# Kernel optimization log

Measured on AMD Instinct MI355X. Metric: run time of the kernel, lower is better.

## Reference

```python
import jax, jax.numpy as jnp
import numpy as np

# Quincunx lattice: coset 0 at integer positions (2i, 2j), coset 1 at (2i+1, 2j+1).
# Stencil offsets in lattice coordinates (coordinate sum even -> on-lattice points).
STENCIL = [(0, 0), (1, 1), (2, 0), (0, 2), (2, 2)]
NEG_INF = -jnp.inf


def _shifted(x, di, dj):
    """Return y with y[..., i, j] = x[..., i+di, j+dj], out-of-range -> -inf."""
    H, W = x.shape[-2], x.shape[-1]
    pi0, pi1 = max(-di, 0), max(di, 0)
    pj0, pj1 = max(-dj, 0), max(dj, 0)
    xp = jnp.pad(x, ((0, 0), (0, 0), (pi0, pi1), (pj0, pj1)),
                 constant_values=NEG_INF)
    si, sj = max(di, 0), max(dj, 0)
    return xp[..., si:si + H, sj:sj + W]


def _pool_coset(own, other, parity):
    """Max over stencil neighbors for points in one coset of the quincunx lattice."""
    out = None
    for (sx, sy) in STENCIL:
        if sx % 2 == 0:  # even offset: stays in the same coset
            cand = _shifted(own, sx // 2, sy // 2)
        else:            # odd offset: crosses to the other coset
            if parity == 0:
                cand = _shifted(other, (sx - 1) // 2, (sy - 1) // 2)
            else:
                cand = _shifted(other, (sx + 1) // 2, (sy + 1) // 2)
        out = cand if out is None else jnp.maximum(out, cand)
    return out


def setup_inputs() -> dict:
    key = jax.random.key(0)
    k0, k1 = jax.random.split(key)
    shape = (4, 32, 512, 512)  # [B, C, H, W] per coset
    return {
        "coset0": jax.random.normal(k0, shape, dtype=jnp.float32),
        "coset1": jax.random.normal(k1, shape, dtype=jnp.float32),
    }


def reference(coset0, coset1):
    out0 = _pool_coset(coset0, coset1, parity=0)
    out1 = _pool_coset(coset1, coset0, parity=1)
    # Stack cosets of the output LatticeTensor: [2, B, C, H, W]
    return jnp.stack([out0, out1], axis=0)
```

## Files before the change

### kernel.cpp

```cpp
#include <hip/hip_runtime.h>
#include <math.h>

#define NEG_INF (-INFINITY)

__global__ __launch_bounds__(256) void quincunx_pool_kernel(
    const float* __restrict__ c0, const float* __restrict__ c1,
    float* __restrict__ out, long N )
{
    const int H = 512, W = 512;
    const int wq = W >> 2;

    long idx = (long)blockIdx.x * blockDim.x + threadIdx.x;
    int j4 = (int)(idx % wq) * 4;
    int i  = (int)((idx / wq) % H);
    long p = idx / ((long)wq * H);

    long base = p * (long)(H * W) + (long)i * W + j4;

    float4 a0 = *(const float4*)(c0 + base);
    float4 b0 = *(const float4*)(c1 + base);

    const bool hasI1 = (i + 1) < H;
    float4 a1, b1;
    if (hasI1) {
        a1 = *(const float4*)(c0 + base + W);
        b1 = *(const float4*)(c1 + base + W);
    } else {
        a1 = make_float4(NEG_INF, NEG_INF, NEG_INF, NEG_INF);
        b1 = a1;
    }

    const bool hasJ = (j4 + 4) < W;
    float a0e = hasJ ? c0[base + 4] : NEG_INF;
    float b0e = hasJ ? c1[base + 4] : NEG_INF;
    float a1e = (hasJ && hasI1) ? c0[base + W + 4] : NEG_INF;
    float b1e = (hasJ && hasI1) ? c1[base + W + 4] : NEG_INF;

    float4 o0, o1;
    o0.x = fmaxf(fmaxf(fmaxf(a0.x, b0.x), fmaxf(a1.x, a0.y)), a1.y);
    o1.x = fmaxf(fmaxf(fmaxf(b0.x, b1.x), fmaxf(b0.y, b1.y)), a1.y);
    o0.y = fmaxf(fmaxf(fmaxf(a0.y, b0.y), fmaxf(a1.y, a0.z)), a1.z);
    o1.y = fmaxf(fmaxf(fmaxf(b0.y, b1.y), fmaxf(b0.z, b1.z)), a1.z);
    o0.z = fmaxf(fmaxf(fmaxf(a0.z, b0.z), fmaxf(a1.z, a0.w)), a1.w);
    o1.z = fmaxf(fmaxf(fmaxf(b0.z, b1.z), fmaxf(b0.w, b1.w)), a1.w);
    o0.w = fmaxf(fmaxf(fmaxf(a0.w, b0.w), fmaxf(a1.w, a0e)), a1e);
    o1.w = fmaxf(fmaxf(fmaxf(b0.w, b1.w), fmaxf(b0e, b1e)), a1e);

    *(float4*)(out + base)     = o0;
    *(float4*)(out + N + base) = o1;
}

extern "C" void kernel_launch(void* const* d_in, const int* in_sizes, int n_in,
                              void* d_out, int out_size, void* d_ws, size_t ws_size,
                              hipStream_t stream) {
    const float* c0 = (const float*)d_in[0];
    const float* c1 = (const float*)d_in[1];
    float* out = (float*)d_out;

    const int H = 512, W = 512;
    long N = (long)in_sizes[0];
    long total_threads = N / 4;
    int threads = 256;
    int blocks = (int)((total_threads + threads - 1) / threads);

    quincunx_pool_kernel<<<blocks, threads, 0, stream>>>(c0, c1, out, N);
}
```

Baseline: 432.1 us.

## Process row strips per thread with register row reuse and lane shuffles

Each thread now walks eight consecutive rows, carrying the lower row into the next iteration so each input row is loaded once per thread instead of twice. Horizontal neighbor elements are obtained with wavefront shuffles instead of extra scalar global loads, with only the last lane loading directly. This cuts redundant global load instructions and cache traffic, at the cost of eight times fewer threads and less memory-level parallelism per element.

```diff
diff --git a/kernel.cpp b/kernel.cpp
--- a/kernel.cpp
+++ b/kernel.cpp
@@ -2,52 +2,72 @@
 #include <math.h>
 
 #define NEG_INF (-INFINITY)
+#define BX 64
+#define BY 4
+#define RPT 8
 
-__global__ __launch_bounds__(256) void quincunx_pool_kernel(
+__global__ __launch_bounds__(BX * BY) void quincunx_pool_kernel(
     const float* __restrict__ c0, const float* __restrict__ c1,
     float* __restrict__ out, long N )
 {
     const int H = 512, W = 512;
-    const int wq = W >> 2;
+    const int tx = threadIdx.x;
+    const int j4 = (blockIdx.x * BX + tx) * 4;
+    const int strip = blockIdx.y * BY + threadIdx.y;
+    const int i0 = strip * RPT;
+    const long plane_base = (long)blockIdx.z * (long)(H * W);
 
-    long idx = (long)blockIdx.x * blockDim.x + threadIdx.x;
-    int j4 = (int)(idx % wq) * 4;
-    int i  = (int)((idx / wq) % H);
-    long p = idx / ((long)wq * H);
+    long off = plane_base + (long)i0 * W + j4;
 
-    long base = p * (long)(H * W) + (long)i * W + j4;
+    const bool edge = (tx == BX - 1);
+    const bool hasJ = (j4 + 4) < W;
 
-    float4 a0 = *(const float4*)(c0 + base);
-    float4 b0 = *(const float4*)(c1 + base);
-
-    const bool hasI1 = (i + 1) < H;
-    float4 a1, b1;
-    if (hasI1) {
-        a1 = *(const float4*)(c0 + base + W);
-        b1 = *(const float4*)(c1 + base + W);
-    } else {
-        a1 = make_float4(NEG_INF, NEG_INF, NEG_INF, NEG_INF);
-        b1 = a1;
+    float4 a0 = *(const float4*)(c0 + off);
+    float4 b0 = *(const float4*)(c1 + off);
+    float a0e = __shfl_down(a0.x, 1, 64);
+    float b0e = __shfl_down(b0.x, 1, 64);
+    if (edge) {
+        a0e = hasJ ? c0[off + 4] : NEG_INF;
+        b0e = hasJ ? c1[off + 4] : NEG_INF;
     }
 
-    const bool hasJ = (j4 + 4) < W;
-    float a0e = hasJ ? c0[base + 4] : NEG_INF;
-    float b0e = hasJ ? c1[base + 4] : NEG_INF;
-    float a1e = (hasJ && hasI1) ? c0[base + W + 4] : NEG_INF;
-    float b1e = (hasJ && hasI1) ? c1[base + W + 4] : NEG_INF;
+    #pragma unroll
+    for (int r = 0; r < RPT; ++r) {
+        const int i1 = i0 + r + 1;
+        float4 a1, b1;
+        float a1e, b1e;
+        if (i1 < H) {
+            a1 = *(const float4*)(c0 + off + W);
+            b1 = *(const float4*)(c1 + off + W);
+            a1e = __shfl_down(a1.x, 1, 64);
+            b1e = __shfl_down(b1.x, 1, 64);
+            if (edge) {
+                a1e = hasJ ? c0[off + W + 4] : NEG_INF;
+                b1e = hasJ ? c1[off + W + 4] : NEG_INF;
+            }
+        } else {
+            a1 = make_float4(NEG_INF, NEG_INF, NEG_INF, NEG_INF);
+            b1 = a1;
+            a1e = NEG_INF;
+            b1e = NEG_INF;
+        }
 
-    float4 o0, o1;
-    o0.x = fmaxf(fmaxf(fmaxf(a0.x, b0.x), fmaxf(a1.x, a0.y)), a1.y);
-    o1.x = fmaxf(fmaxf(fmaxf(b0.x, b1.x), fmaxf(b0.y, b1.y)), a1.y);
-    o0.y = fmaxf(fmaxf(fmaxf(a0.y, b0.y), fmaxf(a1.y, a0.z)), a1.z);
-    o1.y = fmaxf(fmaxf(fmaxf(b0.y, b1.y), fmaxf(b0.z, b1.z)), a1.z);
-    o0.z = fmaxf(fmaxf(fmaxf(a0.z, b0.z), fmaxf(a1.z, a0.w)), a1.w);
-    o1.z = fmaxf(fmaxf(fmaxf(b0.z, b1.z), fmaxf(b0.w, b1.w)), a1.w);
-    o0.w = fmaxf(fmaxf(fmaxf(a0.w, b0.w), fmaxf(a1.w, a0e)), a1e);
-    o1.w = fmaxf(fmaxf(fmaxf(b0.w, b1.w), fmaxf(b0e, b1e)), a1e);
+        float4 o0, o1;
+        o0.x = fmaxf(fmaxf(fmaxf(a0.x, b0.x), fmaxf(a1.x, a0.y)), a1.y);
+        o1.x = fmaxf(fmaxf(fmaxf(b0.x, b1.x), fmaxf(b0.y, b1.y)), a1.y);
+        o0.y = fmaxf(fmaxf(fmaxf(a0.y, b0.y), fmaxf(a1.y, a0.z)), a1.z);
+        o1.y = fmaxf(fmaxf(fmaxf(b0.y, b1.y), fmaxf(b0.z, b1.z)), a1.z);
+        o0.z = fmaxf(fmaxf(fmaxf(a0.z, b0.z), fmaxf(a1.z, a0.w)), a1.w);
+        o1.z = fmaxf(fmaxf(fmaxf(b0.z, b1.z), fmaxf(b0.w, b1.w)), a1.w);
+        o0.w = fmaxf(fmaxf(fmaxf(a0.w, b0.w), fmaxf(a1.w, a0e)), a1e);
+        o1.w = fmaxf(fmaxf(fmaxf(b0.w, b1.w), fmaxf(b0e, b1e)), a1e);
 
-    *(float4*)(out + base)     = o0;
-    *(float4*)(out + N + base) = o1;
+        *(float4*)(out + off)     = o0;
+        *(float4*)(out + N + off) = o1;
+
+        a0 = a1; b0 = b1; a0e = a1e; b0e = b1e;
+        off += W;
+    }
 }
 
 extern "C" void kernel_launch(void* const* d_in, const int* in_sizes, int n_in,
@@ -59,9 +79,12 @@
 
     const int H = 512, W = 512;
     long N = (long)in_sizes[0];
-    long total_threads = N / 4;
-    int threads = 256;
-    int blocks = (int)((total_threads + threads - 1) / threads);
+    int planes = (int)(N / (long)(H * W));
 
-    quincunx_pool_kernel<<<blocks, threads, 0, stream>>>(c0, c1, out, N);
+    dim3 block(BX, BY);
+    dim3 grid(W / (4 * BX),
+              H / (RPT * BY),
+              planes);
+
+    quincunx_pool_kernel<<<grid, block, 0, stream>>>(c0, c1, out, N);
 }
```

Measured after the change: 435.4 us. About the same (+0.8%).
